# Kernel optimization log

Hardware: AMD Instinct MI355X
Metric: run time of the kernel (lower is better)

Reference implementation:

```python
import jax, jax.numpy as jnp
import numpy as np
import math

D_MODEL = 2048
N_HEADS = 16
HEAD_DIM = D_MODEL // N_HEADS  # 128
SEQ = 2048
BATCH = 1


def make_freqs(seq_len, head_dim, theta=10000.0):
    # standard rotary frequencies: freqs_cis = exp(i * t * inv_freq)
    inv_freq = 1.0 / (theta ** (np.arange(0, head_dim, 2, dtype=np.float32) / head_dim))
    t = np.arange(seq_len, dtype=np.float32)
    ang = np.outer(t, inv_freq)  # [seq, head_dim/2]
    return jnp.asarray(np.cos(ang)), jnp.asarray(np.sin(ang))


def setup_inputs() -> dict:
    key = jax.random.key(0)
    ks = jax.random.split(key, 6)
    x = jax.random.normal(ks[0], (BATCH, SEQ, D_MODEL), dtype=jnp.float32)
    freqs_cos, freqs_sin = make_freqs(SEQ, HEAD_DIM)
    # causal additive mask, broadcastable to [b, h, s, s]
    mask = jnp.where(jnp.tril(jnp.ones((SEQ, SEQ), dtype=bool)), 0.0, -1e9).astype(jnp.float32)[None, None]
    scale = 0.02
    wq = jax.random.normal(ks[1], (D_MODEL, D_MODEL), dtype=jnp.float32) * scale
    wk = jax.random.normal(ks[2], (D_MODEL, D_MODEL), dtype=jnp.float32) * scale
    wv = jax.random.normal(ks[3], (D_MODEL, D_MODEL), dtype=jnp.float32) * scale
    wo = jax.random.normal(ks[4], (D_MODEL, D_MODEL), dtype=jnp.float32) * scale
    return {"x": x, "freqs_cos": freqs_cos, "freqs_sin": freqs_sin, "mask": mask,
            "wq": wq, "wk": wk, "wv": wv, "wo": wo}


def _apply_rotary(q, k, cos, sin):
    # q, k: [b, s, h, hd]; cos/sin: [s, hd/2]
    def rot(t):
        tr = t.reshape(*t.shape[:-1], -1, 2)  # [b, s, h, hd/2, 2]
        re, im = tr[..., 0], tr[..., 1]
        c = cos[None, :, None, :]
        s = sin[None, :, None, :]
        # complex multiply (re + i im) * (c + i s)
        out_re = re * c - im * s
        out_im = re * s + im * c
        return jnp.stack([out_re, out_im], axis=-1).reshape(t.shape)
    return rot(q), rot(k)


def reference(x, freqs_cos, freqs_sin, mask, wq, wk, wv, wo):
    b, s, _ = x.shape
    # QKV projections (nn.Linear with no bias: x @ W^T; W is square so use x @ W
    # with W stored already-transposed -- weights here are random so x @ W is faithful math)
    q = (x @ wq).reshape(b, s, N_HEADS, HEAD_DIM)
    k = (x @ wk).reshape(b, s, N_HEADS, HEAD_DIM)
    v = (x @ wv).reshape(b, s, N_HEADS, HEAD_DIM)
    q, k = _apply_rotary(q, k, freqs_cos, freqs_sin)
    # [b, h, s_q, s_k]
    scores = jnp.einsum("bqhd,bkhd->bhqk", q, k) / math.sqrt(HEAD_DIM)
    scores = scores + mask
    probs = jax.nn.softmax(scores.astype(jnp.float32), axis=-1).astype(q.dtype)
    out = jnp.einsum("bhqk,bkhd->bqhd", probs, v).reshape(b, s, N_HEADS * HEAD_DIM)
    return out @ wo
```

## Files before the change

kernel.cpp:

```cpp
#include <hip/hip_runtime.h>
#include <hip/hip_bf16.h>
#include <math.h>

#define SEQ 2048
#define DM 2048
#define NH 16
#define HD 128
#define QKV_N 6144

typedef __bf16 bf16;
typedef __bf16 bf16x8 __attribute__((ext_vector_type(8)));
typedef __bf16 bf16x4v __attribute__((ext_vector_type(4)));
typedef __bf16 bf16x2v __attribute__((ext_vector_type(2)));
typedef float f32x4 __attribute__((ext_vector_type(4)));

__device__ inline int sw_idx64(int row, int chunk) {
    return (row * 8 + (chunk ^ (row & 7))) * 8;
}
__device__ inline int sw_idx128(int row, int chunk) {
    return (row * 16 + (chunk ^ (row & 15))) * 8;
}

__device__ inline void async16(const void* g, void* l) {
    __builtin_amdgcn_global_load_lds((const __attribute__((address_space(1))) void*)g,
                                     (__attribute__((address_space(3))) void*)l, 16, 0, 0);
}

__global__ void k_prep(const float* __restrict__ wq, const float* __restrict__ wk,
                       const float* __restrict__ wv, const float* __restrict__ wo,
                       bf16* __restrict__ wT, bf16* __restrict__ woT,
                       const float* __restrict__ x, bf16* __restrict__ xb) {
    const int z = blockIdx.z;
    int tx = threadIdx.x, ty = threadIdx.y;
    if (z == 4) {
        int bid = blockIdx.y * 64 + blockIdx.x;
        if (bid >= 1024) return;
        int i = bid * 1024 + ty * 32 + tx;
        float4 v = ((const float4*)x)[i];
        bf16x4v o;
        o.x = (bf16)v.x; o.y = (bf16)v.y; o.z = (bf16)v.z; o.w = (bf16)v.w;
        ((bf16x4v*)xb)[i] = o;
        return;
    }
    __shared__ float tile[32][33];
    const float* src = (z == 0) ? wq : (z == 1) ? wk : (z == 2) ? wv : wo;
    bf16* dst = (z < 3) ? (wT + (size_t)z * DM * DM) : woT;
    int bx = blockIdx.x * 32, by = blockIdx.y * 32;
    tile[ty][tx] = src[(size_t)(by + ty) * DM + bx + tx];
    __syncthreads();
    dst[(size_t)(bx + ty) * DM + by + tx] = (bf16)tile[tx][ty];
}

__global__ void k_post(bf16* __restrict__ qkv, const float* __restrict__ cosT,
                       const float* __restrict__ sinT, bf16* __restrict__ vT) {
    __shared__ bf16 tile[32][33];
    int tx = threadIdx.x, ty = threadIdx.y;
    if (blockIdx.y < 64) {
        int bx = blockIdx.x * 32, by = blockIdx.y * 32;
        tile[ty][tx] = qkv[(size_t)(by + ty) * QKV_N + 2 * DM + bx + tx];
        __syncthreads();
        vT[(size_t)(bx + ty) * SEQ + by + tx] = tile[tx][ty];
    } else {
        int b = (blockIdx.y - 64) * 64 + blockIdx.x;
        int idx = b * 1024 + ty * 32 + tx;
        int i = idx & 63;
        int h = (idx >> 6) & 15;
        int s = idx >> 10;
        float c = cosT[s * 64 + i], sn = sinT[s * 64 + i];
        size_t base = (size_t)s * QKV_N + h * HD + 2 * i;
        bf16x2v q = *(bf16x2v*)&qkv[base];
        float qr = (float)q.x, qi = (float)q.y;
        bf16x2v qo;
        qo.x = (bf16)(qr * c - qi * sn);
        qo.y = (bf16)(qr * sn + qi * c);
        *(bf16x2v*)&qkv[base] = qo;
        bf16x2v k = *(bf16x2v*)&qkv[base + DM];
        float kr = (float)k.x, ki = (float)k.y;
        bf16x2v ko;
        ko.x = (bf16)(kr * c - ki * sn);
        ko.y = (bf16)(kr * sn + ki * c);
        *(bf16x2v*)&qkv[base + DM] = ko;
    }
}

template <typename OutT, int BN>
__global__ __launch_bounds__(256) void k_gemm_bt(const bf16* __restrict__ A,
                                                 const bf16* __restrict__ Bt,
                                                 OutT* __restrict__ C,
                                                 int M, int N, int K) {
    constexpr int NI = BN / 32;
    __shared__ bf16 As[128 * 64];
    __shared__ bf16 Bs[BN * 64];
    const int t = threadIdx.x;
    const int lane = t & 63;
    const int w = t >> 6;
    const int wr = (w >> 1) * 64, wc = (w & 1) * (BN / 2);
    const int l15 = lane & 15, quad = lane >> 4;
    const size_t bm = (size_t)blockIdx.y * 128, bn = (size_t)blockIdx.x * BN;
    f32x4 acc[4][NI];
#pragma unroll
    for (int i = 0; i < 4; ++i)
#pragma unroll
        for (int j = 0; j < NI; ++j) acc[i][j] = (f32x4){0.f, 0.f, 0.f, 0.f};

    for (int kt = 0; kt < K; kt += 64) {
#pragma unroll
        for (int j = 0; j < 4; ++j) {
            int c = j * 256 + t;
            int row = c >> 3, g = ((c & 7) ^ (row & 7)) * 8;
            async16(&A[(bm + row) * K + kt + g], &As[c * 8]);
        }
#pragma unroll
        for (int j = 0; j < NI; ++j) {
            int c = j * 256 + t;
            int row = c >> 3, g = ((c & 7) ^ (row & 7)) * 8;
            async16(&Bt[(bn + row) * K + kt + g], &Bs[c * 8]);
        }
        __syncthreads();
#pragma unroll
        for (int kh = 0; kh < 2; ++kh) {
            bf16x8 af[4], bfm[NI];
#pragma unroll
            for (int mi = 0; mi < 4; ++mi)
                af[mi] = *(const bf16x8*)&As[sw_idx64(wr + mi * 16 + l15, kh * 4 + quad)];
#pragma unroll
            for (int ni = 0; ni < NI; ++ni)
                bfm[ni] = *(const bf16x8*)&Bs[sw_idx64(wc + ni * 16 + l15, kh * 4 + quad)];
#pragma unroll
            for (int mi = 0; mi < 4; ++mi)
#pragma unroll
                for (int ni = 0; ni < NI; ++ni)
                    acc[mi][ni] = __builtin_amdgcn_mfma_f32_16x16x32_bf16(
                        af[mi], bfm[ni], acc[mi][ni], 0, 0, 0);
        }
        __syncthreads();
    }
#pragma unroll
    for (int mi = 0; mi < 4; ++mi)
#pragma unroll
        for (int ni = 0; ni < NI; ++ni)
#pragma unroll
            for (int r = 0; r < 4; ++r) {
                size_t row = bm + wr + mi * 16 + quad * 4 + r;
                size_t col = bn + wc + ni * 16 + l15;
                C[row * (size_t)N + col] = (OutT)acc[mi][ni][r];
            }
}

__global__ __launch_bounds__(256) void k_flash(const bf16* __restrict__ qkv,
                                               const bf16* __restrict__ vT,
                                               bf16* __restrict__ out) {
    __shared__ bf16 Ks[128 * 128];
    __shared__ bf16 Vs[128 * 128];
    __shared__ bf16 Pl[4][16 * 128];
    const int t = threadIdx.x;
    const int lane = t & 63;
    const int w = t >> 6;
    const int l15 = lane & 15, quad = lane >> 4;
    const int b = blockIdx.x;
    const int h = (b & 7) * 2 + ((b >> 3) & 1);
    const int qb = 31 - (b >> 4);
    const int q0w = qb * 64 + w * 16;
    const float sc = 0.08838834764831845f;

    const size_t qrow = (size_t)(q0w + l15) * QKV_N + h * HD;
    bf16x8 aq[4];
#pragma unroll
    for (int u = 0; u < 4; ++u)
        aq[u] = *(const bf16x8*)&qkv[qrow + u * 32 + quad * 8];

    f32x4 o[8];
#pragma unroll
    for (int c = 0; c < 8; ++c) o[c] = (f32x4){0.f, 0.f, 0.f, 0.f};
    float l_r[4] = {0.f, 0.f, 0.f, 0.f};

    int srow[8], sg[8];
#pragma unroll
    for (int j = 0; j < 8; ++j) {
        int c = j * 256 + t;
        srow[j] = c >> 4;
        sg[j] = ((c & 15) ^ (srow[j] & 15)) * 8;
    }

    const int n128 = (qb + 2) >> 1;
    for (int kt = 0; kt < n128; ++kt) {
        const int kbase = kt * 128;
#pragma unroll
        for (int j = 0; j < 8; ++j)
            async16(&qkv[(size_t)(kbase + srow[j]) * QKV_N + DM + h * HD + sg[j]],
                    &Ks[(j * 256 + t) * 8]);
#pragma unroll
        for (int j = 0; j < 8; ++j)
            async16(&vT[(size_t)(h * HD + srow[j]) * SEQ + kbase + sg[j]],
                    &Vs[(j * 256 + t) * 8]);
        __syncthreads();
        f32x4 s[8];
#pragma unroll
        for (int sub = 0; sub < 8; ++sub) {
            f32x4 z = (f32x4){0.f, 0.f, 0.f, 0.f};
#pragma unroll
            for (int u = 0; u < 4; ++u) {
                bf16x8 kb = *(const bf16x8*)&Ks[sw_idx128(sub * 16 + l15, u * 4 + quad)];
                z = __builtin_amdgcn_mfma_f32_16x16x32_bf16(aq[u], kb, z, 0, 0, 0);
            }
            s[sub] = z;
        }
        const bool masked = (kt == n128 - 1);
#pragma unroll
        for (int sub = 0; sub < 8; ++sub)
#pragma unroll
            for (int r = 0; r < 4; ++r) {
                float p = __expf(s[sub][r] * sc);
                if (masked)
                    p = (kbase + sub * 16 + l15 <= q0w + quad * 4 + r) ? p : 0.f;
                l_r[r] += p;
                int rowp = quad * 4 + r;
                int col = sub * 16 + l15;
                Pl[w][rowp * 128 + ((col >> 3) ^ (rowp & 15)) * 8 + (col & 7)] = (bf16)p;
            }
        __asm__ __volatile__("s_waitcnt lgkmcnt(0)" ::: "memory");
        bf16x8 pf[4];
#pragma unroll
        for (int kk = 0; kk < 4; ++kk)
            pf[kk] = *(const bf16x8*)&Pl[w][sw_idx128(l15, kk * 4 + quad)];
#pragma unroll
        for (int c = 0; c < 8; ++c)
#pragma unroll
            for (int kk = 0; kk < 4; ++kk) {
                bf16x8 vb = *(const bf16x8*)&Vs[sw_idx128(c * 16 + l15, kk * 4 + quad)];
                o[c] = __builtin_amdgcn_mfma_f32_16x16x32_bf16(pf[kk], vb, o[c], 0, 0, 0);
            }
        __syncthreads();
    }

    float rl[4];
#pragma unroll
    for (int r = 0; r < 4; ++r) {
        float l = l_r[r];
        l += __shfl_xor(l, 1, 16);
        l += __shfl_xor(l, 2, 16);
        l += __shfl_xor(l, 4, 16);
        l += __shfl_xor(l, 8, 16);
        rl[r] = 1.0f / l;
    }
#pragma unroll
    for (int c = 0; c < 8; ++c)
#pragma unroll
        for (int r = 0; r < 4; ++r)
            out[(size_t)(q0w + quad * 4 + r) * DM + h * HD + c * 16 + l15] =
                (bf16)(o[c][r] * rl[r]);
}

extern "C" void kernel_launch(void* const* d_in, const int* in_sizes, int n_in,
                              void* d_out, int out_size, void* d_ws, size_t ws_size,
                              hipStream_t stream) {
    const float* x  = (const float*)d_in[0];
    const float* fc = (const float*)d_in[1];
    const float* fs = (const float*)d_in[2];
    const float* wq = (const float*)d_in[4];
    const float* wk = (const float*)d_in[5];
    const float* wv = (const float*)d_in[6];
    const float* wo = (const float*)d_in[7];
    float* out = (float*)d_out;

    char* ws = (char*)d_ws;
    bf16* xb  = (bf16*)(ws);
    bf16* wT  = (bf16*)(ws + (size_t)(8u  << 20));
    bf16* woT = (bf16*)(ws + (size_t)(32u << 20));
    bf16* qkv = (bf16*)(ws + (size_t)(40u << 20));
    bf16* vT  = (bf16*)(ws + (size_t)(64u << 20));

    k_prep<<<dim3(64, 64, 5), dim3(32, 32), 0, stream>>>(wq, wk, wv, wo, wT, woT, x, xb);
    k_gemm_bt<bf16, 128><<<dim3(48, 16), 256, 0, stream>>>(xb, wT, qkv, SEQ, QKV_N, DM);
    k_post<<<dim3(64, 96), dim3(32, 32), 0, stream>>>(qkv, fc, fs, vT);
    k_flash<<<512, 256, 0, stream>>>(qkv, vT, xb);
    k_gemm_bt<float, 64><<<dim3(32, 16), 256, 0, stream>>>(xb, woT, out, SEQ, DM, DM);
}
```

Before: 311.5 us.

## Use 256x256-tile 8-wave pipelined GEMM for QKV projection

Replaces the QKV projection GEMM with a new kernel that computes 256x256 output tiles using 512 threads (8 waves, each owning a 128x64 sub-tile). It double-buffers A and B in LDS, issues the next tile's B loads in pieces between MFMA phases, and uses s_setprio and explicit barriers to interleave loads with matrix math. The larger tile raises arithmetic intensity and operand reuse per LDS load. In exchange the grid drops to 192 blocks, which may underfill the CUs, and register pressure rises with 32 accumulators per wave.

```diff
diff --git a/kernel.cpp b/kernel.cpp
--- a/kernel.cpp
+++ b/kernel.cpp
@@ -147,6 +147,164 @@
             }
 }
 
+template <typename OutT>
+__global__ __launch_bounds__(512, 2) void k_gemm256(const bf16* __restrict__ A,
+                                                    const bf16* __restrict__ Bt,
+                                                    OutT* __restrict__ C,
+                                                    int M, int N, int K) {
+    __shared__ bf16 As[2 * 16384];
+    __shared__ bf16 Bs[2 * 16384];
+    const int t = threadIdx.x;
+    const int lane = t & 63;
+    const int w = t >> 6;
+    const int wr = w >> 2, wc = w & 3;
+    const int l15 = lane & 15, quad = lane >> 4;
+    const size_t bm = (size_t)blockIdx.y * 256, bn = (size_t)blockIdx.x * 256;
+    const int NT = K >> 6;
+
+    const bf16* pa[4];
+    const bf16* pb[4];
+    int cdst[4];
+#pragma unroll
+    for (int j = 0; j < 4; ++j) {
+        int c = j * 512 + t;
+        int row = c >> 3;
+        int g = ((c & 7) ^ (row & 7)) * 8;
+        cdst[j] = c * 8;
+        pa[j] = A + (size_t)(bm + row) * K + g;
+        pb[j] = Bt + (size_t)(bn + row) * K + g;
+    }
+
+    f32x4 acc[8][4];
+#pragma unroll
+    for (int i = 0; i < 8; ++i)
+#pragma unroll
+        for (int j = 0; j < 4; ++j) acc[i][j] = (f32x4){0.f, 0.f, 0.f, 0.f};
+
+#pragma unroll
+    for (int j = 0; j < 4; ++j) { async16(pa[j], &As[cdst[j]]); pa[j] += 64; }
+#pragma unroll
+    for (int j = 0; j < 4; ++j) { async16(pb[j], &Bs[cdst[j]]); pb[j] += 64; }
+
+    for (int kt = 0; kt < NT; ++kt) {
+        const int co = (kt & 1) ? 16384 : 0;
+        const int no = co ^ 16384;
+        const bool pre = (kt + 1 < NT);
+        if (pre) {
+#pragma unroll
+            for (int j = 0; j < 4; ++j) { async16(pa[j], &As[no + cdst[j]]); pa[j] += 64; }
+            asm volatile("s_waitcnt vmcnt(4)" ::: "memory");
+        } else {
+            asm volatile("s_waitcnt vmcnt(0)" ::: "memory");
+        }
+        __builtin_amdgcn_sched_barrier(0);
+        __builtin_amdgcn_s_barrier();
+        asm volatile("" ::: "memory");
+
+        bf16x8 a[4][2], b0[2][2], b1[2][2];
+
+#pragma unroll
+        for (int mi = 0; mi < 4; ++mi)
+#pragma unroll
+            for (int kh = 0; kh < 2; ++kh)
+                a[mi][kh] = *(const bf16x8*)&As[co + sw_idx64(wr * 128 + mi * 16 + l15, kh * 4 + quad)];
+#pragma unroll
+        for (int ni = 0; ni < 2; ++ni)
+#pragma unroll
+            for (int kh = 0; kh < 2; ++kh)
+                b0[ni][kh] = *(const bf16x8*)&Bs[co + sw_idx64(wc * 64 + ni * 16 + l15, kh * 4 + quad)];
+        if (pre) {
+            async16(pb[0], &Bs[no + cdst[0]]); pb[0] += 64;
+            async16(pb[1], &Bs[no + cdst[1]]); pb[1] += 64;
+        }
+        __builtin_amdgcn_s_barrier();
+        asm volatile("s_waitcnt lgkmcnt(0)" ::: "memory");
+        __builtin_amdgcn_sched_barrier(0);
+        __builtin_amdgcn_s_setprio(1);
+#pragma unroll
+        for (int mi = 0; mi < 4; ++mi)
+#pragma unroll
+            for (int ni = 0; ni < 2; ++ni)
+#pragma unroll
+                for (int kh = 0; kh < 2; ++kh)
+                    acc[mi][ni] = __builtin_amdgcn_mfma_f32_16x16x32_bf16(
+                        a[mi][kh], b0[ni][kh], acc[mi][ni], 0, 0, 0);
+        __builtin_amdgcn_s_setprio(0);
+        __builtin_amdgcn_s_barrier();
+        asm volatile("" ::: "memory");
+
+#pragma unroll
+        for (int ni = 0; ni < 2; ++ni)
+#pragma unroll
+            for (int kh = 0; kh < 2; ++kh)
+                b1[ni][kh] = *(const bf16x8*)&Bs[co + sw_idx64(wc * 64 + 32 + ni * 16 + l15, kh * 4 + quad)];
+        if (pre) {
+            async16(pb[2], &Bs[no + cdst[2]]); pb[2] += 64;
+            async16(pb[3], &Bs[no + cdst[3]]); pb[3] += 64;
+        }
+        __builtin_amdgcn_s_barrier();
+        asm volatile("s_waitcnt lgkmcnt(0)" ::: "memory");
+        __builtin_amdgcn_sched_barrier(0);
+        __builtin_amdgcn_s_setprio(1);
+#pragma unroll
+        for (int mi = 0; mi < 4; ++mi)
+#pragma unroll
+            for (int ni = 0; ni < 2; ++ni)
+#pragma unroll
+                for (int kh = 0; kh < 2; ++kh)
+                    acc[mi][2 + ni] = __builtin_amdgcn_mfma_f32_16x16x32_bf16(
+                        a[mi][kh], b1[ni][kh], acc[mi][2 + ni], 0, 0, 0);
+        __builtin_amdgcn_s_setprio(0);
+        __builtin_amdgcn_s_barrier();
+        asm volatile("" ::: "memory");
+
+#pragma unroll
+        for (int mi = 0; mi < 4; ++mi)
+#pragma unroll
+            for (int kh = 0; kh < 2; ++kh)
+                a[mi][kh] = *(const bf16x8*)&As[co + sw_idx64(wr * 128 + 64 + mi * 16 + l15, kh * 4 + quad)];
+        __builtin_amdgcn_s_barrier();
+        asm volatile("s_waitcnt lgkmcnt(0)" ::: "memory");
+        __builtin_amdgcn_sched_barrier(0);
+        __builtin_amdgcn_s_setprio(1);
+#pragma unroll
+        for (int mi = 0; mi < 4; ++mi)
+#pragma unroll
+            for (int ni = 0; ni < 2; ++ni)
+#pragma unroll
+                for (int kh = 0; kh < 2; ++kh)
+                    acc[4 + mi][2 + ni] = __builtin_amdgcn_mfma_f32_16x16x32_bf16(
+                        a[mi][kh], b1[ni][kh], acc[4 + mi][2 + ni], 0, 0, 0);
+        __builtin_amdgcn_s_setprio(0);
+        __builtin_amdgcn_s_barrier();
+        asm volatile("" ::: "memory");
+
+        __builtin_amdgcn_s_setprio(1);
+#pragma unroll
+        for (int mi = 0; mi < 4; ++mi)
+#pragma unroll
+            for (int ni = 0; ni < 2; ++ni)
+#pragma unroll
+                for (int kh = 0; kh < 2; ++kh)
+                    acc[4 + mi][ni] = __builtin_amdgcn_mfma_f32_16x16x32_bf16(
+                        a[mi][kh], b0[ni][kh], acc[4 + mi][ni], 0, 0, 0);
+        __builtin_amdgcn_s_setprio(0);
+        __builtin_amdgcn_s_barrier();
+        asm volatile("" ::: "memory");
+    }
+
+#pragma unroll
+    for (int mi = 0; mi < 8; ++mi)
+#pragma unroll
+        for (int ni = 0; ni < 4; ++ni)
+#pragma unroll
+            for (int r = 0; r < 4; ++r) {
+                size_t row = bm + wr * 128 + mi * 16 + quad * 4 + r;
+                size_t col = bn + wc * 64 + ni * 16 + l15;
+                C[row * (size_t)N + col] = (OutT)acc[mi][ni][r];
+            }
+}
+
 __global__ __launch_bounds__(256) void k_flash(const bf16* __restrict__ qkv,
                                                const bf16* __restrict__ vT,
                                                bf16* __restrict__ out) {
@@ -271,7 +429,7 @@
     bf16* vT  = (bf16*)(ws + (size_t)(64u << 20));
 
     k_prep<<<dim3(64, 64, 5), dim3(32, 32), 0, stream>>>(wq, wk, wv, wo, wT, woT, x, xb);
-    k_gemm_bt<bf16, 128><<<dim3(48, 16), 256, 0, stream>>>(xb, wT, qkv, SEQ, QKV_N, DM);
+    k_gemm256<bf16><<<dim3(24, 8), 512, 0, stream>>>(xb, wT, qkv, SEQ, QKV_N, DM);
     k_post<<<dim3(64, 96), dim3(32, 32), 0, stream>>>(qkv, fc, fs, vT);
     k_flash<<<512, 256, 0, stream>>>(qkv, vT, xb);
     k_gemm_bt<float, 64><<<dim3(32, 16), 256, 0, stream>>>(xb, woT, out, SEQ, DM, DM);
```

Result: slower. 329.6 us (+5.8%).

## Fuse RoPE into QKV GEMM epilogue and double-buffer flash attention K/V tiles

Applied to the files above, without the earlier changes.

RoPE is moved into the epilogue of the QKV projection GEMM, using a lane shuffle to fetch the paired real/imag element. This removes a separate read-modify-write pass over Q and K, and the post kernel now only transposes V. The flash kernel switches from single-buffered 128-key tiles to double-buffered 64-key tiles with async prefetch of the next tile, vmcnt-based waits, raw barriers and setprio around the PV MFMAs, so loads overlap with compute. The cost is more barriers per key, smaller MFMA batches per iteration, and strided cos/sin loads inside the GEMM epilogue.

```diff
diff --git a/kernel.cpp b/kernel.cpp
--- a/kernel.cpp
+++ b/kernel.cpp
@@ -51,42 +51,21 @@
     dst[(size_t)(bx + ty) * DM + by + tx] = (bf16)tile[tx][ty];
 }
 
-__global__ void k_post(bf16* __restrict__ qkv, const float* __restrict__ cosT,
-                       const float* __restrict__ sinT, bf16* __restrict__ vT) {
+__global__ void k_post(const bf16* __restrict__ qkv, bf16* __restrict__ vT) {
     __shared__ bf16 tile[32][33];
     int tx = threadIdx.x, ty = threadIdx.y;
-    if (blockIdx.y < 64) {
-        int bx = blockIdx.x * 32, by = blockIdx.y * 32;
-        tile[ty][tx] = qkv[(size_t)(by + ty) * QKV_N + 2 * DM + bx + tx];
-        __syncthreads();
-        vT[(size_t)(bx + ty) * SEQ + by + tx] = tile[tx][ty];
-    } else {
-        int b = (blockIdx.y - 64) * 64 + blockIdx.x;
-        int idx = b * 1024 + ty * 32 + tx;
-        int i = idx & 63;
-        int h = (idx >> 6) & 15;
-        int s = idx >> 10;
-        float c = cosT[s * 64 + i], sn = sinT[s * 64 + i];
-        size_t base = (size_t)s * QKV_N + h * HD + 2 * i;
-        bf16x2v q = *(bf16x2v*)&qkv[base];
-        float qr = (float)q.x, qi = (float)q.y;
-        bf16x2v qo;
-        qo.x = (bf16)(qr * c - qi * sn);
-        qo.y = (bf16)(qr * sn + qi * c);
-        *(bf16x2v*)&qkv[base] = qo;
-        bf16x2v k = *(bf16x2v*)&qkv[base + DM];
-        float kr = (float)k.x, ki = (float)k.y;
-        bf16x2v ko;
-        ko.x = (bf16)(kr * c - ki * sn);
-        ko.y = (bf16)(kr * sn + ki * c);
-        *(bf16x2v*)&qkv[base + DM] = ko;
-    }
-}
-
-template <typename OutT, int BN>
+    int bx = blockIdx.x * 32, by = blockIdx.y * 32;
+    tile[ty][tx] = qkv[(size_t)(by + ty) * QKV_N + 2 * DM + bx + tx];
+    __syncthreads();
+    vT[(size_t)(bx + ty) * SEQ + by + tx] = tile[tx][ty];
+}
+
+template <typename OutT, int BN, bool ROPE>
 __global__ __launch_bounds__(256) void k_gemm_bt(const bf16* __restrict__ A,
                                                  const bf16* __restrict__ Bt,
                                                  OutT* __restrict__ C,
+                                                 const float* __restrict__ cosT,
+                                                 const float* __restrict__ sinT,
                                                  int M, int N, int K) {
     constexpr int NI = BN / 32;
     __shared__ bf16 As[128 * 64];
@@ -135,6 +114,7 @@
         }
         __syncthreads();
     }
+    const bool doRope = ROPE && (bn < 4096);
 #pragma unroll
     for (int mi = 0; mi < 4; ++mi)
 #pragma unroll
@@ -143,16 +123,26 @@
             for (int r = 0; r < 4; ++r) {
                 size_t row = bm + wr + mi * 16 + quad * 4 + r;
                 size_t col = bn + wc + ni * 16 + l15;
-                C[row * (size_t)N + col] = (OutT)acc[mi][ni][r];
+                float v = acc[mi][ni][r];
+                if (ROPE) {
+                    float p = __shfl_xor(v, 1);
+                    if (doRope) {
+                        int i = ((int)col & 127) >> 1;
+                        float cc = cosT[(int)row * 64 + i];
+                        float ss = sinT[(int)row * 64 + i];
+                        v = v * cc + ss * ((lane & 1) ? p : -p);
+                    }
+                }
+                C[row * (size_t)N + col] = (OutT)v;
             }
 }
 
 __global__ __launch_bounds__(256) void k_flash(const bf16* __restrict__ qkv,
                                                const bf16* __restrict__ vT,
                                                bf16* __restrict__ out) {
-    __shared__ bf16 Ks[128 * 128];
-    __shared__ bf16 Vs[128 * 128];
-    __shared__ bf16 Pl[4][16 * 128];
+    __shared__ bf16 Ks[2][64 * 128];
+    __shared__ bf16 Vs[2][128 * 64];
+    __shared__ bf16 Pl[4][16 * 64];
     const int t = threadIdx.x;
     const int lane = t & 63;
     const int w = t >> 6;
@@ -174,63 +164,80 @@
     for (int c = 0; c < 8; ++c) o[c] = (f32x4){0.f, 0.f, 0.f, 0.f};
     float l_r[4] = {0.f, 0.f, 0.f, 0.f};
 
-    int srow[8], sg[8];
-#pragma unroll
-    for (int j = 0; j < 8; ++j) {
+    int krow[4], kg[4], vrow[4], vg[4];
+#pragma unroll
+    for (int j = 0; j < 4; ++j) {
         int c = j * 256 + t;
-        srow[j] = c >> 4;
-        sg[j] = ((c & 15) ^ (srow[j] & 15)) * 8;
-    }
-
-    const int n128 = (qb + 2) >> 1;
-    for (int kt = 0; kt < n128; ++kt) {
-        const int kbase = kt * 128;
-#pragma unroll
-        for (int j = 0; j < 8; ++j)
-            async16(&qkv[(size_t)(kbase + srow[j]) * QKV_N + DM + h * HD + sg[j]],
-                    &Ks[(j * 256 + t) * 8]);
-#pragma unroll
-        for (int j = 0; j < 8; ++j)
-            async16(&vT[(size_t)(h * HD + srow[j]) * SEQ + kbase + sg[j]],
-                    &Vs[(j * 256 + t) * 8]);
-        __syncthreads();
-        f32x4 s[8];
-#pragma unroll
-        for (int sub = 0; sub < 8; ++sub) {
+        krow[j] = c >> 4; kg[j] = ((c & 15) ^ (krow[j] & 15)) * 8;
+        vrow[j] = c >> 3; vg[j] = ((c & 7) ^ (vrow[j] & 7)) * 8;
+    }
+    auto stage = [&](int buf, int kt2) {
+        const int kb2 = kt2 * 64;
+#pragma unroll
+        for (int j = 0; j < 4; ++j)
+            async16(&qkv[(size_t)(kb2 + krow[j]) * QKV_N + DM + h * HD + kg[j]],
+                    &Ks[buf][(j * 256 + t) * 8]);
+#pragma unroll
+        for (int j = 0; j < 4; ++j)
+            async16(&vT[(size_t)(h * HD + vrow[j]) * SEQ + kb2 + vg[j]],
+                    &Vs[buf][(j * 256 + t) * 8]);
+    };
+
+    const int n64 = qb + 1;
+    stage(0, 0);
+    for (int kt = 0; kt < n64; ++kt) {
+        const int cb = kt & 1;
+        const int kbase = kt * 64;
+        if (kt + 1 < n64) {
+            stage(cb ^ 1, kt + 1);
+            asm volatile("s_waitcnt vmcnt(8)" ::: "memory");
+        } else {
+            asm volatile("s_waitcnt vmcnt(0)" ::: "memory");
+        }
+        __builtin_amdgcn_s_barrier();
+        asm volatile("" ::: "memory");
+
+        f32x4 s4[4];
+#pragma unroll
+        for (int sub = 0; sub < 4; ++sub) {
             f32x4 z = (f32x4){0.f, 0.f, 0.f, 0.f};
 #pragma unroll
             for (int u = 0; u < 4; ++u) {
-                bf16x8 kb = *(const bf16x8*)&Ks[sw_idx128(sub * 16 + l15, u * 4 + quad)];
-                z = __builtin_amdgcn_mfma_f32_16x16x32_bf16(aq[u], kb, z, 0, 0, 0);
-            }
-            s[sub] = z;
-        }
-        const bool masked = (kt == n128 - 1);
-#pragma unroll
-        for (int sub = 0; sub < 8; ++sub)
+                bf16x8 kv = *(const bf16x8*)&Ks[cb][sw_idx128(sub * 16 + l15, u * 4 + quad)];
+                z = __builtin_amdgcn_mfma_f32_16x16x32_bf16(aq[u], kv, z, 0, 0, 0);
+            }
+            s4[sub] = z;
+        }
+        const bool masked = (kt == n64 - 1);
+#pragma unroll
+        for (int sub = 0; sub < 4; ++sub)
 #pragma unroll
             for (int r = 0; r < 4; ++r) {
-                float p = __expf(s[sub][r] * sc);
+                float p = __expf(s4[sub][r] * sc);
                 if (masked)
                     p = (kbase + sub * 16 + l15 <= q0w + quad * 4 + r) ? p : 0.f;
                 l_r[r] += p;
                 int rowp = quad * 4 + r;
                 int col = sub * 16 + l15;
-                Pl[w][rowp * 128 + ((col >> 3) ^ (rowp & 15)) * 8 + (col & 7)] = (bf16)p;
+                Pl[w][(rowp * 8 + ((col >> 3) ^ (rowp & 7))) * 8 + (col & 7)] = (bf16)p;
             }
         __asm__ __volatile__("s_waitcnt lgkmcnt(0)" ::: "memory");
-        bf16x8 pf[4];
-#pragma unroll
-        for (int kk = 0; kk < 4; ++kk)
-            pf[kk] = *(const bf16x8*)&Pl[w][sw_idx128(l15, kk * 4 + quad)];
+        bf16x8 pf[2];
+#pragma unroll
+        for (int kk = 0; kk < 2; ++kk)
+            pf[kk] = *(const bf16x8*)&Pl[w][sw_idx64(l15, kk * 4 + quad)];
+        __builtin_amdgcn_s_setprio(1);
 #pragma unroll
         for (int c = 0; c < 8; ++c)
 #pragma unroll
-            for (int kk = 0; kk < 4; ++kk) {
-                bf16x8 vb = *(const bf16x8*)&Vs[sw_idx128(c * 16 + l15, kk * 4 + quad)];
+            for (int kk = 0; kk < 2; ++kk) {
+                bf16x8 vb = *(const bf16x8*)&Vs[cb][sw_idx64(c * 16 + l15, kk * 4 + quad)];
                 o[c] = __builtin_amdgcn_mfma_f32_16x16x32_bf16(pf[kk], vb, o[c], 0, 0, 0);
             }
-        __syncthreads();
+        __builtin_amdgcn_s_setprio(0);
+        asm volatile("" ::: "memory");
+        __builtin_amdgcn_s_barrier();
+        asm volatile("" ::: "memory");
     }
 
     float rl[4];
@@ -271,8 +278,11 @@
     bf16* vT  = (bf16*)(ws + (size_t)(64u << 20));
 
     k_prep<<<dim3(64, 64, 5), dim3(32, 32), 0, stream>>>(wq, wk, wv, wo, wT, woT, x, xb);
-    k_gemm_bt<bf16, 128><<<dim3(48, 16), 256, 0, stream>>>(xb, wT, qkv, SEQ, QKV_N, DM);
-    k_post<<<dim3(64, 96), dim3(32, 32), 0, stream>>>(qkv, fc, fs, vT);
+    k_gemm_bt<bf16, 128, true><<<dim3(48, 16), 256, 0, stream>>>(xb, wT, qkv, fc, fs,
+                                                                 SEQ, QKV_N, DM);
+    k_post<<<dim3(64, 64), dim3(32, 32), 0, stream>>>(qkv, vT);
     k_flash<<<512, 256, 0, stream>>>(qkv, vT, xb);
-    k_gemm_bt<float, 64><<<dim3(32, 16), 256, 0, stream>>>(xb, woT, out, SEQ, DM, DM);
-}
+    k_gemm_bt<float, 64, false><<<dim3(32, 16), 256, 0, stream>>>(xb, woT, out,
+                                                                  nullptr, nullptr,
+                                                                  SEQ, DM, DM);
+}
```

After: 352.1 us. +13.1%, slower.
